# Performance work log

Measured on AMD Instinct MI355X. Metric: run time of the kernel, lower is better.

Reference implementation:

```python
import jax, jax.numpy as jnp
import numpy as np

N_NODE, N_USER = 100000, 30000
N_REL, N_BASIS = 8, 30
EMB, OUT = 32, 32
E = 1600000
BATCH = 16384
H1, H2, H3 = 64, 32, 16
NEG_SLOPE = 0.2


def setup_inputs() -> dict:
    key = jax.random.key(0)
    ks = jax.random.split(key, 20)
    g = lambda k, shape: jax.random.normal(k, shape, dtype=jnp.float32) * 0.05
    inp = {
        "x_ids": jnp.arange(N_NODE, dtype=jnp.int64 if jax.config.jax_enable_x64 else jnp.int32),
        "edge_index": jax.random.randint(ks[0], (2, E), 0, N_NODE),
        "edge_type": jax.random.randint(ks[1], (E,), 0, N_REL),
        "users": jax.random.randint(ks[2], (BATCH,), 0, N_USER),
        "bundles": jax.random.randint(ks[3], (BATCH,), 0, N_NODE),
        # parameters
        "emb": g(ks[4], (N_NODE, EMB)),
        "basis": g(ks[5], (N_BASIS, EMB, OUT)),
        "weight": g(ks[6], (N_REL, N_BASIS)),
        "att": g(ks[7], (N_REL, 2 * OUT)),
        "root": g(ks[8], (EMB, OUT)),
        "bias": jnp.zeros((OUT,), jnp.float32),
        "W1": g(ks[9], (2 * OUT, H1)), "b1": jnp.zeros((H1,), jnp.float32),
        "W2": g(ks[10], (H1, H2)), "b2": jnp.zeros((H2,), jnp.float32),
        "W3": g(ks[11], (H2, H3)), "b3": jnp.zeros((H3,), jnp.float32),
        "Wo": g(ks[12], (H3, 1)), "bo": jnp.zeros((1,), jnp.float32),
    }
    return inp


def _tgcn_fwd(x_ids, edge_index, edge_type, users, bundles,
              emb, basis, weight, att, root, bias,
              W1, b1, W2, b2, W3, b3, Wo, bo):
    N = emb.shape[0]
    R = weight.shape[0]
    O = basis.shape[2]
    x = emb[x_ids]                                   # (N, F) embedding lookup
    # basis decomposition: (R, F, O)
    w = (weight @ basis.reshape(N_BASIS, -1)).reshape(R, EMB, O)
    # transform every node under every relation once, then gather per edge
    xh = jnp.einsum('nf,rfo->nro', x, w)             # (N, R, O)
    src, dst = edge_index[0], edge_index[1]          # j (source), i (target)
    h_i = xh[dst, edge_type]                         # (E, O)
    h_j = xh[src, edge_type]                         # (E, O)
    a = att[edge_type]                               # (E, 2O)
    alpha = (h_i * a[:, :O]).sum(-1) + (h_j * a[:, O:]).sum(-1)
    alpha = jax.nn.leaky_relu(alpha, NEG_SLOPE)
    # segment softmax keyed by (target node, relation)
    seg_key = dst * R + edge_type
    n_seg = N * R
    amax = jax.ops.segment_max(alpha, seg_key, num_segments=n_seg)
    ex = jnp.exp(alpha - amax[seg_key])
    denom = jax.ops.segment_sum(ex, seg_key, num_segments=n_seg)
    alpha = ex / (denom[seg_key] + 1e-16)
    # scatter-add weighted messages into target nodes
    agg = jax.ops.segment_sum(h_j * alpha[:, None], dst, num_segments=N)
    h = jax.nn.relu(agg + x @ root + bias)           # update + ReLU
    z = jnp.concatenate([h[users], h[bundles]], axis=1)  # (B, 2O)
    z = jax.nn.relu(z @ W1 + b1)
    z = jax.nn.relu(z @ W2 + b2)
    z = jax.nn.relu(z @ W3 + b3)
    return z @ Wo + bo                               # (B, 1) logits


def reference(x_ids, edge_index, edge_type, users, bundles,
              emb, basis, weight, att, root, bias,
              W1, b1, W2, b2, W3, b3, Wo, bo):
    return _tgcn_fwd(x_ids, edge_index, edge_type, users, bundles,
                     emb, basis, weight, att, root, bias,
                     W1, b1, W2, b2, W3, b3, Wo, bo)
```

## Files before the change

kernel.cpp:

```cpp
#include <hip/hip_runtime.h>
#include <hip/hip_bf16.h>

#define N_NODE 100000
#define N_REL  8
#define EMB    32
#define OUT    32
#define N_BASIS 30
#define E_EDGE 1600000
#define BATCH  16384
#define H1 64
#define H2 32
#define H3 16
#define NEG_SLOPE 0.2f

#define BSH   8
#define NBKT  391
#define BCAP  5120
#define PCH   2048

#define K5T   128


__global__ __launch_bounds__(256) void k0f(const float* __restrict__ weight,
                                           const float* __restrict__ basis,
                                           const float* __restrict__ att,
                                           float* __restrict__ w,
                                           float* __restrict__ wa,
                                           unsigned* __restrict__ bcnt) {
    __shared__ float wl[N_REL * EMB * OUT];
    int t = threadIdx.x;
    for (int i = t; i < N_REL * EMB * OUT; i += 256) {
        int r = i >> 10, fo = i & 1023;
        float acc = 0.f;
        #pragma unroll
        for (int b = 0; b < N_BASIS; b++)
            acc = fmaf(weight[r * N_BASIS + b], basis[b * (EMB * OUT) + fo], acc);
        wl[i] = acc;
        w[i] = acc;
    }
    __syncthreads();
    for (int i = t; i < 512; i += 256) {
        int which = i >> 8, rf = i & 255, r = rf >> 5, f = rf & 31;
        const float* wrow = wl + (r * 32 + f) * 32;
        const float* arow = att + r * 64 + which * 32;
        float acc = 0.f;
        #pragma unroll
        for (int o = 0; o < 32; o++) acc = fmaf(wrow[o], arow[o], acc);
        wa[i] = acc;
    }
    for (int i = t; i < NBKT; i += 256) bcnt[i] = 0;
}

__global__ __launch_bounds__(256, 4) void k1_transform(const float* __restrict__ emb,
                                                       const float* __restrict__ w,
                                                       unsigned short* __restrict__ xh) {
    const int t = threadIdx.x;
    const int o = t & 31;
    const int r = t >> 5;

    float wc[EMB];
    #pragma unroll
    for (int f = 0; f < EMB; f++) wc[f] = w[(r * EMB + f) * OUT + o];
    #pragma unroll
    for (int f = 0; f < EMB; f++) asm volatile("" : "+v"(wc[f]));

    for (int n0 = blockIdx.x * 4; n0 < N_NODE; n0 += gridDim.x * 4) {
        const float* __restrict__ x0 = emb + (size_t)(n0 + 0) * EMB;
        const float* __restrict__ x1 = emb + (size_t)(n0 + 1) * EMB;
        const float* __restrict__ x2 = emb + (size_t)(n0 + 2) * EMB;
        const float* __restrict__ x3 = emb + (size_t)(n0 + 3) * EMB;

        float a0 = 0.f, a1 = 0.f, a2 = 0.f, a3 = 0.f;
        #pragma unroll
        for (int f = 0; f < EMB; f++) {
            a0 = fmaf(x0[f], wc[f], a0);
            a1 = fmaf(x1[f], wc[f], a1);
            a2 = fmaf(x2[f], wc[f], a2);
            a3 = fmaf(x3[f], wc[f], a3);
        }
        __hip_bfloat16 b0 = __float2bfloat16(a0);
        __hip_bfloat16 b1 = __float2bfloat16(a1);
        __hip_bfloat16 b2 = __float2bfloat16(a2);
        __hip_bfloat16 b3 = __float2bfloat16(a3);
        xh[(size_t)(n0 + 0) * 256 + t] = *(unsigned short*)&b0;
        xh[(size_t)(n0 + 1) * 256 + t] = *(unsigned short*)&b1;
        xh[(size_t)(n0 + 2) * 256 + t] = *(unsigned short*)&b2;
        xh[(size_t)(n0 + 3) * 256 + t] = *(unsigned short*)&b3;
    }
}

__global__ __launch_bounds__(256) void k_pi(const float* __restrict__ emb,
                                            const float* __restrict__ wa,
                                            const float* __restrict__ root,
                                            const float* __restrict__ bias,
                                            float* __restrict__ p_i,
                                            float* __restrict__ p_j,
                                            float* __restrict__ agg) {
    __shared__ float rs[EMB * OUT];
    __shared__ float bs[OUT];
    __shared__ float wis[256], wjs[256];
    int t = threadIdx.x;
    for (int i = t; i < EMB * OUT; i += 256) rs[i] = root[i];
    if (t < OUT) bs[t] = bias[t];
    for (int i = t; i < 512; i += 256) {
        int which = i >> 8, r = (i >> 5) & 7, f = i & 31;
        float v = wa[i];
        if (which == 0) wis[f * 8 + r] = v; else wjs[f * 8 + r] = v;
    }
    __syncthreads();
    int tg = blockIdx.x * 256 + t;
    int n = tg >> 5, o = tg & 31;
    const float4* xr4 = (const float4*)(emb + (size_t)n * EMB);
    float xf[EMB];
    #pragma unroll
    for (int c = 0; c < 8; c++) {
        float4 xv = xr4[c];
        xf[4 * c + 0] = xv.x; xf[4 * c + 1] = xv.y;
        xf[4 * c + 2] = xv.z; xf[4 * c + 3] = xv.w;
    }
    float a = bs[o];
    #pragma unroll
    for (int f = 0; f < EMB; f++) a = fmaf(xf[f], rs[f * 32 + o], a);
    agg[tg] = a;
    if (o < N_REL) {
        float ai = 0.f, aj = 0.f;
        #pragma unroll
        for (int f = 0; f < EMB; f++) {
            ai = fmaf(xf[f], wis[f * 8 + o], ai);
            aj = fmaf(xf[f], wjs[f * 8 + o], aj);
        }
        p_i[n * N_REL + o] = ai;
        p_j[n * N_REL + o] = aj;
    }
}

__global__ __launch_bounds__(256) void k_part(const int* __restrict__ src,
                                              const int* __restrict__ dst,
                                              const int* __restrict__ et,
                                              unsigned* __restrict__ bcnt,
                                              unsigned* __restrict__ part) {
    __shared__ unsigned long long stage[PCH];
    __shared__ unsigned hist[NBKT], lbase[NBKT], lcur[NBKT], gbase[NBKT];
    __shared__ unsigned sc[256];
    int t = threadIdx.x;
    for (int i = t; i < NBKT; i += 256) hist[i] = 0;
    __syncthreads();
    int beg = blockIdx.x * PCH, end = min(beg + PCH, E_EDGE);
    int n = end - beg;
    int ng = n >> 2;
    int g0 = t, g1 = t + 256;
    bool has0 = g0 < ng, has1 = g1 < ng;
    int4 s0v = {}, d0v = {}, e0v = {}, s1v = {}, d1v = {}, e1v = {};
    if (has0) {
        s0v = *(const int4*)&src[beg + 4 * g0];
        d0v = *(const int4*)&dst[beg + 4 * g0];
        e0v = *(const int4*)&et[beg + 4 * g0];
    }
    if (has1) {
        s1v = *(const int4*)&src[beg + 4 * g1];
        d1v = *(const int4*)&dst[beg + 4 * g1];
        e1v = *(const int4*)&et[beg + 4 * g1];
    }
    if (has0) {
        atomicAdd(&hist[(unsigned)d0v.x >> BSH], 1u);
        atomicAdd(&hist[(unsigned)d0v.y >> BSH], 1u);
        atomicAdd(&hist[(unsigned)d0v.z >> BSH], 1u);
        atomicAdd(&hist[(unsigned)d0v.w >> BSH], 1u);
    }
    if (has1) {
        atomicAdd(&hist[(unsigned)d1v.x >> BSH], 1u);
        atomicAdd(&hist[(unsigned)d1v.y >> BSH], 1u);
        atomicAdd(&hist[(unsigned)d1v.z >> BSH], 1u);
        atomicAdd(&hist[(unsigned)d1v.w >> BSH], 1u);
    }
    __syncthreads();
    unsigned v0 = (2 * t < NBKT) ? hist[2 * t] : 0u;
    unsigned v1 = (2 * t + 1 < NBKT) ? hist[2 * t + 1] : 0u;
    unsigned s = v0 + v1;
    sc[t] = s;
    __syncthreads();
    for (int off = 1; off < 256; off <<= 1) {
        unsigned y = (t >= off) ? sc[t - off] : 0u;
        __syncthreads();
        sc[t] += y;
        __syncthreads();
    }
    unsigned ex = sc[t] - s;
    if (2 * t < NBKT)     { lbase[2 * t] = ex;          lcur[2 * t] = ex; }
    if (2 * t + 1 < NBKT) { lbase[2 * t + 1] = ex + v0; lcur[2 * t + 1] = ex + v0; }
    __syncthreads();
    #define K_PART_STAGE(dd, ss, ee) do {                                   \
        unsigned b_ = (unsigned)(dd) >> BSH;                                \
        unsigned ent_ = ((unsigned)((dd) & 255) << 20)                      \
                      | ((unsigned)(ss) << 3) | (unsigned)(ee);             \
        unsigned pos_ = atomicAdd(&lcur[b_], 1u);                           \
        stage[pos_] = ((unsigned long long)b_ << 32) | ent_; } while (0)
    if (has0) {
        K_PART_STAGE(d0v.x, s0v.x, e0v.x);
        K_PART_STAGE(d0v.y, s0v.y, e0v.y);
        K_PART_STAGE(d0v.z, s0v.z, e0v.z);
        K_PART_STAGE(d0v.w, s0v.w, e0v.w);
    }
    if (has1) {
        K_PART_STAGE(d1v.x, s1v.x, e1v.x);
        K_PART_STAGE(d1v.y, s1v.y, e1v.y);
        K_PART_STAGE(d1v.z, s1v.z, e1v.z);
        K_PART_STAGE(d1v.w, s1v.w, e1v.w);
    }
    #undef K_PART_STAGE
    __syncthreads();
    for (int i = t; i < NBKT; i += 256)
        if (hist[i]) gbase[i] = atomicAdd(&bcnt[i], hist[i]);
    __syncthreads();
    for (int i = t; i < n; i += 256) {
        unsigned long long s64 = stage[i];
        unsigned b = (unsigned)(s64 >> 32);
        unsigned ent = (unsigned)s64;
        part[b * BCAP + gbase[b] + (i - lbase[b])] = ent;
    }
}

__global__ __launch_bounds__(256) void k_sort(const unsigned* __restrict__ bcnt,
                                              const unsigned* __restrict__ part,
                                              int* __restrict__ payload,
                                              int* __restrict__ begp,
                                              int* __restrict__ endp) {
    __shared__ unsigned ent[BCAP];
    __shared__ unsigned ent2[BCAP];
    __shared__ unsigned hist[256], dbase[256], dcur[256];
    __shared__ unsigned sc[256];
    int t = threadIdx.x;
    int b = blockIdx.x;
    unsigned s0 = (unsigned)b * BCAP;
    int n = (int)bcnt[b];
    if (n > BCAP) n = BCAP;
    hist[t] = 0;
    __syncthreads();
    int n4 = n & ~3;
    for (int i = 4 * t; i < n4; i += 1024) {
        uint4 e4 = *(const uint4*)&part[s0 + i];
        ent[i + 0] = e4.x; atomicAdd(&hist[e4.x >> 20], 1u);
        ent[i + 1] = e4.y; atomicAdd(&hist[e4.y >> 20], 1u);
        ent[i + 2] = e4.z; atomicAdd(&hist[e4.z >> 20], 1u);
        ent[i + 3] = e4.w; atomicAdd(&hist[e4.w >> 20], 1u);
    }
    for (int i = n4 + t; i < n; i += 256) {
        unsigned e = part[s0 + i];
        ent[i] = e;
        atomicAdd(&hist[e >> 20], 1u);
    }
    __syncthreads();
    unsigned v = hist[t];
    sc[t] = v;
    __syncthreads();
    for (int off = 1; off < 256; off <<= 1) {
        unsigned y = (t >= off) ? sc[t - off] : 0u;
        __syncthreads();
        sc[t] += y;
        __syncthreads();
    }
    unsigned ex = sc[t] - v;
    dbase[t] = ex;
    dcur[t] = ex;
    __syncthreads();
    int d = (b << BSH) + t;
    if (d < N_NODE) {
        begp[d] = (int)(s0 + dbase[t]);
        endp[d] = (int)(s0 + dbase[t] + hist[t]);
    }
    for (int i = t; i < n; i += 256) {
        unsigned e = ent[i];
        unsigned pos = atomicAdd(&dcur[e >> 20], 1u);
        ent2[pos] = e & 0xFFFFFu;
    }
    __syncthreads();
    for (int i = 4 * t; i < n4; i += 1024) {
        uint4 o4 = { ent2[i + 0], ent2[i + 1], ent2[i + 2], ent2[i + 3] };
        *(uint4*)&payload[s0 + i] = o4;
    }
    for (int i = n4 + t; i < n; i += 256) payload[s0 + i] = (int)ent2[i];
}

__global__ __launch_bounds__(256) void k_agg(const int* __restrict__ begp,
                                             const int* __restrict__ endp,
                                             const int* __restrict__ payload,
                                             const float* __restrict__ p_i,
                                             const float* __restrict__ p_j,
                                             const unsigned short* __restrict__ xh,
                                             float* __restrict__ agg,
                                             int d0, int d1) {
    int d = d0 + blockIdx.x * 4 + (threadIdx.x >> 6);
    if (d >= d1) return;
    const int lane = threadIdx.x & 63;
    const int h = lane >> 5;
    const int o = lane & 31;
    const int beg = begp[d], end = endp[d];
    const int cnt = end - beg;
    if (cnt == 0) return;

    float pid[8];
    #pragma unroll
    for (int k = 0; k < 8; k++) pid[k] = p_i[(d << 3) | k];

    if (cnt <= 64) {
        int sr = 0, r = 0; float ev = 0.f;
        if (lane < cnt) {
            sr = payload[beg + lane];
            r = sr & 7;
            float pi = pid[0];
            #pragma unroll
            for (int k = 1; k < 8; k++) pi = (r == k) ? pid[k] : pi;
            float a = pi + p_j[sr];
            a = (a >= 0.f) ? a : NEG_SLOPE * a;
            ev = __expf(a);
        }
        float sex[8];
        #pragma unroll
        for (int k = 0; k < 8; k++) sex[k] = (r == k) ? ev : 0.f;
        #pragma unroll
        for (int k = 0; k < 8; k++) {
            #pragma unroll
            for (int m = 1; m <= 32; m <<= 1) sex[k] += __shfl_xor(sex[k], m, 64);
        }
        float de = sex[0];
        #pragma unroll
        for (int k = 1; k < 8; k++) de = (r == k) ? sex[k] : de;
        float al = ev / (de + 1e-16f);

        float w0 = 0.f, w1 = 0.f, w2 = 0.f, w3 = 0.f;
        for (int j0 = 0; j0 < cnt; j0 += 8) {
            float b0 = __shfl(al, j0 + h,     64);
            float b1 = __shfl(al, j0 + 2 + h, 64);
            float b2 = __shfl(al, j0 + 4 + h, 64);
            float b3 = __shfl(al, j0 + 6 + h, 64);
            int t0 = payload[beg + j0 + h]     & 0xFFFFF;
            int t1 = payload[beg + j0 + 2 + h] & 0xFFFFF;
            int t2 = payload[beg + j0 + 4 + h] & 0xFFFFF;
            int t3 = payload[beg + j0 + 6 + h] & 0xFFFFF;
            float x0 = __uint_as_float((unsigned)xh[((unsigned)t0 << 5) + o] << 16);
            float x1 = __uint_as_float((unsigned)xh[((unsigned)t1 << 5) + o] << 16);
            float x2 = __uint_as_float((unsigned)xh[((unsigned)t2 << 5) + o] << 16);
            float x3 = __uint_as_float((unsigned)xh[((unsigned)t3 << 5) + o] << 16);
            w0 = fmaf(b0, x0, w0); w1 = fmaf(b1, x1, w1);
            w2 = fmaf(b2, x2, w2); w3 = fmaf(b3, x3, w3);
        }
        float vv = (w0 + w1) + (w2 + w3);
        vv += __shfl_xor(vv, 32, 64);
        if (h == 0) agg[(size_t)d * OUT + o] += vv;
        return;
    }

    float sex[8] = {0.f,0.f,0.f,0.f,0.f,0.f,0.f,0.f};
    for (int i = beg + lane; i < end; i += 64) {
        int sr = payload[i];
        int r = sr & 7;
        float pi = pid[0];
        #pragma unroll
        for (int k = 1; k < 8; k++) pi = (r == k) ? pid[k] : pi;
        float a = pi + p_j[sr];
        a = (a >= 0.f) ? a : NEG_SLOPE * a;
        float ev = __expf(a);
        #pragma unroll
        for (int k = 0; k < 8; k++) sex[k] += (r == k) ? ev : 0.f;
    }
    #pragma unroll
    for (int k = 0; k < 8; k++) {
        #pragma unroll
        for (int m = 1; m <= 32; m <<= 1) sex[k] += __shfl_xor(sex[k], m, 64);
    }
    float v0 = 0.f;
    for (int c = beg; c < end; c += 64) {
        int i = c + lane;
        int sr = 0; float al = 0.f;
        if (i < end) {
            sr = payload[i];
            int r = sr & 7;
            float pi = pid[0];
            #pragma unroll
            for (int k = 1; k < 8; k++) pi = (r == k) ? pid[k] : pi;
            float a = pi + p_j[sr];
            a = (a >= 0.f) ? a : NEG_SLOPE * a;
            float ev = __expf(a);
            float de = sex[0];
            #pragma unroll
            for (int k = 1; k < 8; k++) de = (r == k) ? sex[k] : de;
            al = ev / (de + 1e-16f);
        }
        int m = min(64, end - c);
        for (int j0 = 0; j0 < m; j0 += 2) {
            int e0 = j0 + h;
            float a0 = __shfl(al, e0, 64); int s0 = __shfl(sr, e0, 64);
            if (e0 < m) {
                float xv = __uint_as_float((unsigned)xh[((unsigned)s0 << 5) + o] << 16);
                v0 = fmaf(a0, xv, v0);
            }
        }
    }
    float vv = v0;
    vv += __shfl_xor(vv, 32, 64);
    if (h == 0) agg[(size_t)d * OUT + o] += vv;
}

__global__ __launch_bounds__(K5T, 1) void k5_mlp(const int* __restrict__ users,
                                                 const int* __restrict__ bundles,
                                                 const float* __restrict__ agg,
                                                 const float* __restrict__ W1,
                                                 const float* __restrict__ b1,
                                                 const float* __restrict__ W2,
                                                 const float* __restrict__ b2,
                                                 const float* __restrict__ W3,
                                                 const float* __restrict__ b3,
                                                 const float* __restrict__ Wo,
                                                 const float* __restrict__ bo,
                                                 float* __restrict__ out) {
    __shared__ float4 W1s[2 * OUT * H1 / 4];
    __shared__ float4 W2s[H1 * H2 / 4];
    __shared__ float4 W3s[H2 * H3 / 4];
    __shared__ float b1s[H1], b2s[H2], b3s[H3], Wos[H3];
    __shared__ float bos;
    __shared__ float zs[K5T * 65];
    __shared__ float h1s[K5T * 65];
    const int t = threadIdx.x;

    const float4* W14 = (const float4*)W1;
    const float4* W24 = (const float4*)W2;
    const float4* W34 = (const float4*)W3;
    for (int i = t; i < 1024; i += K5T) W1s[i] = W14[i];
    for (int i = t; i < 512; i += K5T) W2s[i] = W24[i];
    for (int i = t; i < 128; i += K5T) W3s[i] = W34[i];
    if (t < H1) b1s[t] = b1[t];
    if (t < H2) b2s[t] = b2[t];
    if (t < H3) { b3s[t] = b3[t]; Wos[t] = Wo[t]; }
    if (t == 0) bos = bo[0];

    const int item = blockIdx.x * K5T + t;
    const int u = users[item], v = bundles[item];
    const float4* av = (const float4*)agg;
    float* zrow = &zs[t * 65];
    float* h1row = &h1s[t * 65];

    #pragma unroll
    for (int c = 0; c < 8; c++) {
        float4 x = av[(size_t)u * 8 + c];
        zrow[4 * c + 0] = fmaxf(x.x, 0.f); zrow[4 * c + 1] = fmaxf(x.y, 0.f);
        zrow[4 * c + 2] = fmaxf(x.z, 0.f); zrow[4 * c + 3] = fmaxf(x.w, 0.f);
    }
    #pragma unroll
    for (int c = 0; c < 8; c++) {
        float4 x = av[(size_t)v * 8 + c];
        zrow[32 + 4 * c + 0] = fmaxf(x.x, 0.f); zrow[32 + 4 * c + 1] = fmaxf(x.y, 0.f);
        zrow[32 + 4 * c + 2] = fmaxf(x.z, 0.f); zrow[32 + 4 * c + 3] = fmaxf(x.w, 0.f);
    }
    __syncthreads();

    #pragma unroll 4
    for (int j4 = 0; j4 < 16; j4++) {
        float a0 = b1s[4 * j4 + 0], a1 = b1s[4 * j4 + 1];
        float a2 = b1s[4 * j4 + 2], a3 = b1s[4 * j4 + 3];
        #pragma unroll 16
        for (int k = 0; k < 2 * OUT; k++) {
            float zk = zrow[k];
            float4 wv = W1s[k * 16 + j4];
            a0 = fmaf(zk, wv.x, a0); a1 = fmaf(zk, wv.y, a1);
            a2 = fmaf(zk, wv.z, a2); a3 = fmaf(zk, wv.w, a3);
        }
        h1row[4 * j4 + 0] = fmaxf(a0, 0.f); h1row[4 * j4 + 1] = fmaxf(a1, 0.f);
        h1row[4 * j4 + 2] = fmaxf(a2, 0.f); h1row[4 * j4 + 3] = fmaxf(a3, 0.f);
    }

    #pragma unroll 4
    for (int j4 = 0; j4 < 8; j4++) {
        float a0 = b2s[4 * j4 + 0], a1 = b2s[4 * j4 + 1];
        float a2 = b2s[4 * j4 + 2], a3 = b2s[4 * j4 + 3];
        #pragma unroll 16
        for (int k = 0; k < H1; k++) {
            float hk = h1row[k];
            float4 wv = W2s[k * 8 + j4];
            a0 = fmaf(hk, wv.x, a0); a1 = fmaf(hk, wv.y, a1);
            a2 = fmaf(hk, wv.z, a2); a3 = fmaf(hk, wv.w, a3);
        }
        zrow[4 * j4 + 0] = fmaxf(a0, 0.f); zrow[4 * j4 + 1] = fmaxf(a1, 0.f);
        zrow[4 * j4 + 2] = fmaxf(a2, 0.f); zrow[4 * j4 + 3] = fmaxf(a3, 0.f);
    }

    float h3v[16];
    #pragma unroll
    for (int j4 = 0; j4 < 4; j4++) {
        float a0 = b3s[4 * j4 + 0], a1 = b3s[4 * j4 + 1];
        float a2 = b3s[4 * j4 + 2], a3 = b3s[4 * j4 + 3];
        #pragma unroll 16
        for (int k = 0; k < H2; k++) {
            float hk = zrow[k];
            float4 wv = W3s[k * 4 + j4];
            a0 = fmaf(hk, wv.x, a0); a1 = fmaf(hk, wv.y, a1);
            a2 = fmaf(hk, wv.z, a2); a3 = fmaf(hk, wv.w, a3);
        }
        h3v[4 * j4 + 0] = fmaxf(a0, 0.f); h3v[4 * j4 + 1] = fmaxf(a1, 0.f);
        h3v[4 * j4 + 2] = fmaxf(a2, 0.f); h3v[4 * j4 + 3] = fmaxf(a3, 0.f);
    }

    float acc = bos;
    #pragma unroll
    for (int k = 0; k < H3; k++) acc = fmaf(h3v[k], Wos[k], acc);
    out[item] = acc;
}

extern "C" void kernel_launch(void* const* d_in, const int* in_sizes, int n_in,
                              void* d_out, int out_size, void* d_ws, size_t ws_size,
                              hipStream_t stream) {
    (void)in_sizes; (void)n_in; (void)out_size; (void)ws_size;
    const int*   eidx   = (const int*)d_in[1];
    const int*   etype  = (const int*)d_in[2];
    const int*   users  = (const int*)d_in[3];
    const int*   bund   = (const int*)d_in[4];
    const float* emb    = (const float*)d_in[5];
    const float* basis  = (const float*)d_in[6];
    const float* weight = (const float*)d_in[7];
    const float* att    = (const float*)d_in[8];
    const float* root   = (const float*)d_in[9];
    const float* bias   = (const float*)d_in[10];
    const float* W1 = (const float*)d_in[11]; const float* b1 = (const float*)d_in[12];
    const float* W2 = (const float*)d_in[13]; const float* b2 = (const float*)d_in[14];
    const float* W3 = (const float*)d_in[15]; const float* b3 = (const float*)d_in[16];
    const float* Wo = (const float*)d_in[17]; const float* bo = (const float*)d_in[18];
    float* out = (float*)d_out;

    const int* src = eidx;
    const int* dst = eidx + E_EDGE;

    float* ws       = (float*)d_ws;
    float* w        = ws;
    float* wa       = w + N_REL * EMB * OUT;
    unsigned short* xh = (unsigned short*)(wa + 512);
    float* p_i      = (float*)(xh + (size_t)N_NODE * 256);
    float* p_j      = p_i + N_NODE * N_REL;
    float* agg      = p_j + N_NODE * N_REL;
    int*   payload  = (int*)(agg + (long)N_NODE * OUT);
    int*   begp     = payload + NBKT * BCAP;
    int*   endp     = begp + N_NODE;
    unsigned* bcnt  = (unsigned*)(endp + N_NODE);
    unsigned* part  = (unsigned*)agg;

    k0f<<<1, 256, 0, stream>>>(weight, basis, att, w, wa, bcnt);
    k_part<<<(E_EDGE + PCH - 1) / PCH, 256, 0, stream>>>(src, dst, etype, bcnt, part);
    k_sort<<<NBKT, 256, 0, stream>>>(bcnt, part, payload, begp, endp);
    k1_transform<<<2048, 256, 0, stream>>>(emb, w, xh);
    k_pi<<<(N_NODE * OUT) / 256, 256, 0, stream>>>(emb, wa, root, bias,
                                                   p_i, p_j, agg);
    k_agg<<<12500, 256, 0, stream>>>(begp, endp, payload, p_i, p_j, xh, agg,
                                     0, 50000);
    k_agg<<<12500, 256, 0, stream>>>(begp, endp, payload, p_i, p_j, xh, agg,
                                     50000, 100000);
    k5_mlp<<<BATCH / K5T, K5T, 0, stream>>>(users, bund, agg, W1, b1, W2, b2, W3, b3,
                                            Wo, bo, out);
}
```

Baseline: 335.4 us.

## Fuse node transform, attention projections and root update into one kernel

Result: slower. 349.4 us (+4.1%).

```diff
diff --git a/kernel.cpp b/kernel.cpp
--- a/kernel.cpp
+++ b/kernel.cpp
@@ -20,6 +20,9 @@
 
 #define K5T   128
 
+#define NPB   16
+#define K1GRID 2048
+
 
 __global__ __launch_bounds__(256) void k0f(const float* __restrict__ weight,
                                            const float* __restrict__ basis,
@@ -51,9 +54,20 @@
     for (int i = t; i < NBKT; i += 256) bcnt[i] = 0;
 }
 
-__global__ __launch_bounds__(256, 4) void k1_transform(const float* __restrict__ emb,
-                                                       const float* __restrict__ w,
-                                                       unsigned short* __restrict__ xh) {
+__global__ __launch_bounds__(256) void k1x(const float* __restrict__ emb,
+                                           const float* __restrict__ w,
+                                           const float* __restrict__ att,
+                                           const float* __restrict__ root,
+                                           const float* __restrict__ bias,
+                                           unsigned short* __restrict__ xh,
+                                           float* __restrict__ p_i,
+                                           float* __restrict__ p_j,
+                                           float* __restrict__ agg) {
+    __shared__ float xs[2][NPB * EMB];
+    __shared__ float atts[N_REL * 2 * OUT];
+    __shared__ float rootsT[OUT * 34];
+    __shared__ float biass[OUT];
+
     const int t = threadIdx.x;
     const int o = t & 31;
     const int r = t >> 5;
@@ -64,73 +78,66 @@
     #pragma unroll
     for (int f = 0; f < EMB; f++) asm volatile("" : "+v"(wc[f]));
 
-    for (int n0 = blockIdx.x * 4; n0 < N_NODE; n0 += gridDim.x * 4) {
-        const float* __restrict__ x0 = emb + (size_t)(n0 + 0) * EMB;
-        const float* __restrict__ x1 = emb + (size_t)(n0 + 1) * EMB;
-        const float* __restrict__ x2 = emb + (size_t)(n0 + 2) * EMB;
-        const float* __restrict__ x3 = emb + (size_t)(n0 + 3) * EMB;
-
-        float a0 = 0.f, a1 = 0.f, a2 = 0.f, a3 = 0.f;
-        #pragma unroll
-        for (int f = 0; f < EMB; f++) {
-            a0 = fmaf(x0[f], wc[f], a0);
-            a1 = fmaf(x1[f], wc[f], a1);
-            a2 = fmaf(x2[f], wc[f], a2);
-            a3 = fmaf(x3[f], wc[f], a3);
-        }
-        __hip_bfloat16 b0 = __float2bfloat16(a0);
-        __hip_bfloat16 b1 = __float2bfloat16(a1);
-        __hip_bfloat16 b2 = __float2bfloat16(a2);
-        __hip_bfloat16 b3 = __float2bfloat16(a3);
-        xh[(size_t)(n0 + 0) * 256 + t] = *(unsigned short*)&b0;
-        xh[(size_t)(n0 + 1) * 256 + t] = *(unsigned short*)&b1;
-        xh[(size_t)(n0 + 2) * 256 + t] = *(unsigned short*)&b2;
-        xh[(size_t)(n0 + 3) * 256 + t] = *(unsigned short*)&b3;
-    }
-}
-
-__global__ __launch_bounds__(256) void k_pi(const float* __restrict__ emb,
-                                            const float* __restrict__ wa,
-                                            const float* __restrict__ root,
-                                            const float* __restrict__ bias,
-                                            float* __restrict__ p_i,
-                                            float* __restrict__ p_j,
-                                            float* __restrict__ agg) {
-    __shared__ float rs[EMB * OUT];
-    __shared__ float bs[OUT];
-    __shared__ float wis[256], wjs[256];
-    int t = threadIdx.x;
-    for (int i = t; i < EMB * OUT; i += 256) rs[i] = root[i];
-    if (t < OUT) bs[t] = bias[t];
-    for (int i = t; i < 512; i += 256) {
-        int which = i >> 8, r = (i >> 5) & 7, f = i & 31;
-        float v = wa[i];
-        if (which == 0) wis[f * 8 + r] = v; else wjs[f * 8 + r] = v;
-    }
-    __syncthreads();
-    int tg = blockIdx.x * 256 + t;
-    int n = tg >> 5, o = tg & 31;
-    const float4* xr4 = (const float4*)(emb + (size_t)n * EMB);
-    float xf[EMB];
-    #pragma unroll
-    for (int c = 0; c < 8; c++) {
-        float4 xv = xr4[c];
-        xf[4 * c + 0] = xv.x; xf[4 * c + 1] = xv.y;
-        xf[4 * c + 2] = xv.z; xf[4 * c + 3] = xv.w;
-    }
-    float a = bs[o];
-    #pragma unroll
-    for (int f = 0; f < EMB; f++) a = fmaf(xf[f], rs[f * 32 + o], a);
-    agg[tg] = a;
-    if (o < N_REL) {
-        float ai = 0.f, aj = 0.f;
-        #pragma unroll
-        for (int f = 0; f < EMB; f++) {
-            ai = fmaf(xf[f], wis[f * 8 + o], ai);
-            aj = fmaf(xf[f], wjs[f * 8 + o], aj);
-        }
-        p_i[n * N_REL + o] = ai;
-        p_j[n * N_REL + o] = aj;
+    for (int i = t; i < 512; i += 256) atts[i] = att[i];
+    for (int i = t; i < EMB * OUT; i += 256) {
+        int f = i >> 5, oo = i & 31;
+        rootsT[oo * 34 + f] = root[i];
+    }
+    if (t < OUT) biass[t] = bias[t];
+
+    int n0 = blockIdx.x * NPB;
+    ((float2*)xs[0])[t] = ((const float2*)(emb + (size_t)n0 * EMB))[t];
+    __syncthreads();
+
+    const float aco = atts[r * 64 + o];
+    const float acj = atts[r * 64 + 32 + o];
+
+    int buf = 0;
+    for (; n0 < N_NODE; n0 += K1GRID * NPB) {
+        int n1 = n0 + K1GRID * NPB;
+        if (n1 < N_NODE)
+            ((float2*)xs[buf ^ 1])[t] = ((const float2*)(emb + (size_t)n1 * EMB))[t];
+
+        #pragma unroll 4
+        for (int k = 0; k < NPB; k++) {
+            const float4* xr = (const float4*)&xs[buf][k * EMB];
+            float a = 0.f;
+            #pragma unroll
+            for (int c = 0; c < 8; c++) {
+                float4 xv = xr[c];
+                a = fmaf(xv.x, wc[4 * c + 0], a);
+                a = fmaf(xv.y, wc[4 * c + 1], a);
+                a = fmaf(xv.z, wc[4 * c + 2], a);
+                a = fmaf(xv.w, wc[4 * c + 3], a);
+            }
+            __hip_bfloat16 hb = __float2bfloat16(a);
+            xh[(size_t)(n0 + k) * 256 + t] = *(unsigned short*)&hb;
+
+            float ai = a * aco, aj = a * acj;
+            #pragma unroll
+            for (int m = 1; m <= 16; m <<= 1) {
+                ai += __shfl_xor(ai, m, 64);
+                aj += __shfl_xor(aj, m, 64);
+            }
+            if (o == 0)      p_i[(n0 + k) * N_REL + r] = ai;
+            else if (o == 1) p_j[(n0 + k) * N_REL + r] = aj;
+
+            if (r == (k & 7)) {
+                float g = biass[o];
+                const float* rt = &rootsT[o * 34];
+                #pragma unroll
+                for (int c = 0; c < 8; c++) {
+                    float4 xv = xr[c];
+                    float2 r0 = *(const float2*)&rt[4 * c];
+                    float2 r1 = *(const float2*)&rt[4 * c + 2];
+                    g = fmaf(xv.x, r0.x, g); g = fmaf(xv.y, r0.y, g);
+                    g = fmaf(xv.z, r1.x, g); g = fmaf(xv.w, r1.y, g);
+                }
+                agg[(size_t)(n0 + k) * OUT + o] = g;
+            }
+        }
+        __syncthreads();
+        buf ^= 1;
     }
 }
 
@@ -544,9 +551,7 @@
     k0f<<<1, 256, 0, stream>>>(weight, basis, att, w, wa, bcnt);
     k_part<<<(E_EDGE + PCH - 1) / PCH, 256, 0, stream>>>(src, dst, etype, bcnt, part);
     k_sort<<<NBKT, 256, 0, stream>>>(bcnt, part, payload, begp, endp);
-    k1_transform<<<2048, 256, 0, stream>>>(emb, w, xh);
-    k_pi<<<(N_NODE * OUT) / 256, 256, 0, stream>>>(emb, wa, root, bias,
-                                                   p_i, p_j, agg);
+    k1x<<<K1GRID, 256, 0, stream>>>(emb, w, att, root, bias, xh, p_i, p_j, agg);
     k_agg<<<12500, 256, 0, stream>>>(begp, endp, payload, p_i, p_j, xh, agg,
                                      0, 50000);
     k_agg<<<12500, 256, 0, stream>>>(begp, endp, payload, p_i, p_j, xh, agg,
```
